# Kernel optimization log

Measured on AMD Instinct MI355X. Metric: run time of the kernel, lower is better.

## Reference

```python
import jax, jax.numpy as jnp
import numpy as np

N, E, B = 50000, 800000, 64
IN_C, HID, HEADS = 128, 64, 4
NEG_SLOPE = 0.2


def _gat_layer(x, src, dst, W, a_src, a_dst, bias, heads, out_c, concat):
    # x: [N, F_in] -> h: [N, heads, out_c]
    h = (x @ W).reshape(-1, heads, out_c)
    alpha_src = jnp.sum(h * a_src[None], axis=-1)  # [N, heads]
    alpha_dst = jnp.sum(h * a_dst[None], axis=-1)  # [N, heads]
    e = jax.nn.leaky_relu(alpha_src[src] + alpha_dst[dst], NEG_SLOPE)  # [Etot, heads]
    # segment softmax over incoming edges of each destination node
    m = jax.lax.stop_gradient(jax.ops.segment_max(e, dst, num_segments=N))
    m = jnp.where(jnp.isfinite(m), m, 0.0)
    ex = jnp.exp(e - m[dst])
    denom = jax.ops.segment_sum(ex, dst, num_segments=N)
    alpha = ex / jnp.maximum(denom[dst], 1e-16)
    msg = h[src] * alpha[:, :, None]  # [Etot, heads, out_c]
    out = jax.ops.segment_sum(msg, dst, num_segments=N)  # [N, heads, out_c]
    if concat:
        return out.reshape(-1, heads * out_c) + bias
    return out.mean(axis=1) + bias


def setup_inputs() -> dict:
    key = jax.random.key(0)
    ks = jax.random.split(key, 16)
    g = lambda k, shp, fan: jax.random.normal(k, shp, jnp.float32) * (1.0 / np.sqrt(fan))
    return {
        "x": jax.random.normal(ks[0], (N, IN_C), jnp.float32),
        "edge_index": jax.random.randint(ks[1], (2, E), 0, N, jnp.int64),
        "batch": jnp.sort(jax.random.randint(ks[2], (N,), 0, B, jnp.int64)),
        "W1": g(ks[3], (IN_C, HEADS * HID), IN_C),
        "as1": g(ks[4], (HEADS, HID), HID),
        "ad1": g(ks[5], (HEADS, HID), HID),
        "b1": jnp.zeros((HEADS * HID,), jnp.float32),
        "W2": g(ks[6], (HEADS * HID, HEADS * HID), HEADS * HID),
        "as2": g(ks[7], (HEADS, HID), HID),
        "ad2": g(ks[8], (HEADS, HID), HID),
        "b2": jnp.zeros((HID,), jnp.float32),
        "Wm1": g(ks[9], (HID, HID), HID),
        "bm1": jnp.zeros((HID,), jnp.float32),
        "Wm2": g(ks[10], (HID, 1), HID),
        "bm2": jnp.zeros((1,), jnp.float32),
    }


def reference(x, edge_index, batch, W1, as1, ad1, b1, W2, as2, ad2, b2, Wm1, bm1, Wm2, bm2):
    # add self loops (PyG GATConv default)
    loops = jnp.arange(N, dtype=edge_index.dtype)
    src = jnp.concatenate([edge_index[0], loops])
    dst = jnp.concatenate([edge_index[1], loops])
    h = _gat_layer(x, src, dst, W1, as1, ad1, b1, HEADS, HID, concat=True)
    h = jax.nn.relu(h)
    h = _gat_layer(h, src, dst, W2, as2, ad2, b2, HEADS, HID, concat=False)
    # global mean pool over graphs
    counts = jax.ops.segment_sum(jnp.ones((N,), h.dtype), batch, num_segments=B)
    pooled = jax.ops.segment_sum(h, batch, num_segments=B) / jnp.maximum(counts, 1.0)[:, None]
    # graph MLP
    out = jax.nn.relu(pooled @ Wm1 + bm1) @ Wm2 + bm2  # [B, 1]
    return out
```

## Files before the change

### kernel.cpp

```cpp
#include <hip/hip_runtime.h>
#include <hip/hip_bf16.h>

#define N_NODES 50000
#define N_EDGES 800000
#define ETOT    (N_EDGES + N_NODES)
#define NB      64
#define IN_C    128
#define HID     64
#define HEADS   4
#define F1      (HEADS * HID)
#define NEG     0.2f
#define SCAN_NBLK ((N_NODES + 255) / 256)

typedef __attribute__((ext_vector_type(8))) short  short8v;
typedef __attribute__((ext_vector_type(4))) float  float4v;

__device__ __forceinline__ float lrelu(float x) { return x >= 0.f ? x : NEG * x; }

__device__ __forceinline__ unsigned short f2bf(float f) {
    unsigned u = __float_as_uint(f);
    u += 0x7FFFu + ((u >> 16) & 1u);
    return (unsigned short)(u >> 16);
}
__device__ __forceinline__ float bf2f(unsigned short h) {
    return __uint_as_float(((unsigned)h) << 16);
}

__device__ __forceinline__ int wf_idx(int k, int n) {
    return (((k >> 5) * 16 + (n >> 4)) << 9) + (((k >> 3) & 3) << 7) + ((n & 15) << 3) + (k & 7);
}

__global__ void deg_kernel(const int* __restrict__ ei, int* __restrict__ deg,
                           const float* __restrict__ W1,
                           unsigned short* __restrict__ W1h, unsigned short* __restrict__ W1l,
                           const float* __restrict__ W2,
                           unsigned short* __restrict__ W2h, unsigned short* __restrict__ W2l) {
    int e = blockIdx.x * 256 + threadIdx.x;
    const int N1 = IN_C * 256;
    if (e < N1) {
        int k = e >> 8, n = e & 255;
        float v = W1[e];
        unsigned short h = f2bf(v);
        int idx = wf_idx(k, n);
        W1h[idx] = h;
        W1l[idx] = f2bf(v - bf2f(h));
    } else if (e < N1 + F1 * 256) {
        int j = e - N1;
        int k = j >> 8, n = j & 255;
        float v = W2[j];
        unsigned short h = f2bf(v);
        int idx = wf_idx(k, n);
        W2h[idx] = h;
        W2l[idx] = f2bf(v - bf2f(h));
    }
    if (e >= ETOT) return;
    int d = (e < N_EDGES) ? ei[N_EDGES + e] : (e - N_EDGES);
    atomicAdd(&deg[d], 1);
}

__global__ void scan1_kernel(const int* __restrict__ deg, int* __restrict__ part) {
    __shared__ int sh[256];
    int t = threadIdx.x;
    int i = blockIdx.x * 256 + t;
    sh[t] = (i < N_NODES) ? deg[i] : 0;
    __syncthreads();
    #pragma unroll
    for (int o = 128; o; o >>= 1) {
        if (t < o) sh[t] += sh[t + o];
        __syncthreads();
    }
    if (t == 0) part[blockIdx.x] = sh[0];
}

__global__ void scan2_kernel(int* __restrict__ part, int* __restrict__ off) {
    __shared__ int sh[256];
    int t = threadIdx.x;
    int v = (t < SCAN_NBLK) ? part[t] : 0;
    sh[t] = v;
    __syncthreads();
    #pragma unroll
    for (int o = 1; o < 256; o <<= 1) {
        int u = (t >= o) ? sh[t - o] : 0;
        __syncthreads();
        sh[t] += u;
        __syncthreads();
    }
    if (t < SCAN_NBLK) part[t] = sh[t] - v;
    if (t == 255) off[N_NODES] = sh[255];
}

__global__ void scan3_kernel(int* __restrict__ deg, const int* __restrict__ part,
                             int* __restrict__ off) {
    __shared__ int sh[256];
    int t = threadIdx.x;
    int i = blockIdx.x * 256 + t;
    int v = (i < N_NODES) ? deg[i] : 0;
    sh[t] = v;
    __syncthreads();
    #pragma unroll
    for (int o = 1; o < 256; o <<= 1) {
        int u = (t >= o) ? sh[t - o] : 0;
        __syncthreads();
        sh[t] += u;
        __syncthreads();
    }
    if (i < N_NODES) {
        off[i] = part[blockIdx.x] + sh[t] - v;
        deg[i] = 0;
    }
}

__global__ void scatter_kernel(const int* __restrict__ ei, const int* __restrict__ off,
                               int* __restrict__ cursor, int* __restrict__ esrc) {
    int e = blockIdx.x * 256 + threadIdx.x;
    if (e >= ETOT) return;
    int s, d;
    if (e < N_EDGES) { s = ei[e]; d = ei[N_EDGES + e]; }
    else             { s = d = e - N_EDGES; }
    int pos = off[d] + atomicAdd(&cursor[d], 1);
    esrc[pos] = s;
}

template <bool SPLIT_A, int K>
__global__ __launch_bounds__(256) void gemm_mfma(const float* __restrict__ Af32,
                                                 const unsigned short* __restrict__ Abg,
                                                 const unsigned short* __restrict__ Wfh,
                                                 const unsigned short* __restrict__ Wfl,
                                                 const float* __restrict__ a_s,
                                                 const float* __restrict__ a_d,
                                                 unsigned short* __restrict__ Cb,
                                                 float* __restrict__ asrcO,
                                                 float* __restrict__ adstO,
                                                 int M) {
    __shared__ float smc[32][260];
    int t  = threadIdx.x;
    int m0 = blockIdx.x * 64;
    int w  = t >> 6, l = t & 63;
    int lr = l & 15, lk = (l >> 4) * 8;

    float asv[4], adv[4];
    #pragma unroll
    for (int nf = 0; nf < 4; ++nf) {
        asv[nf] = a_s[w * 64 + nf * 16 + lr];
        adv[nf] = a_d[w * 64 + nf * 16 + lr];
    }

    float4v acc[4][4];
    #pragma unroll
    for (int mf = 0; mf < 4; ++mf)
        #pragma unroll
        for (int nf = 0; nf < 4; ++nf)
            acc[mf][nf] = (float4v){0.f, 0.f, 0.f, 0.f};

    constexpr int KB = K / 32;
    #pragma unroll 2
    for (int kb = 0; kb < KB; ++kb) {
        short8v b_hf[4], b_lf[4];
        #pragma unroll
        for (int nf = 0; nf < 4; ++nf) {
            size_t bidx = (size_t)((kb * 16 + w * 4 + nf) * 512 + l * 8);
            b_hf[nf] = *(const short8v*)&Wfh[bidx];
            b_lf[nf] = *(const short8v*)&Wfl[bidx];
        }
        short8v a_f[4];
        #pragma unroll
        for (int mf = 0; mf < 4; ++mf) {
            int gr = m0 + mf * 16 + lr;
            if (SPLIT_A) {
                float4 v0 = make_float4(0.f, 0.f, 0.f, 0.f), v1 = v0;
                if (gr < M) {
                    const float* ap = &Af32[(size_t)gr * K + kb * 32 + lk];
                    v0 = *(const float4*)ap;
                    v1 = *(const float4*)(ap + 4);
                }
                short8v a;
                a[0] = (short)f2bf(v0.x); a[1] = (short)f2bf(v0.y);
                a[2] = (short)f2bf(v0.z); a[3] = (short)f2bf(v0.w);
                a[4] = (short)f2bf(v1.x); a[5] = (short)f2bf(v1.y);
                a[6] = (short)f2bf(v1.z); a[7] = (short)f2bf(v1.w);
                a_f[mf] = a;
            } else {
                short8v a = {0,0,0,0,0,0,0,0};
                if (gr < M) a = *(const short8v*)&Abg[(size_t)gr * K + kb * 32 + lk];
                a_f[mf] = a;
            }
        }
        #pragma unroll
        for (int mf = 0; mf < 4; ++mf)
            #pragma unroll
            for (int nf = 0; nf < 4; ++nf) {
                acc[mf][nf] = __builtin_amdgcn_mfma_f32_16x16x32_bf16(a_f[mf], b_hf[nf], acc[mf][nf], 0, 0, 0);
                acc[mf][nf] = __builtin_amdgcn_mfma_f32_16x16x32_bf16(a_f[mf], b_lf[nf], acc[mf][nf], 0, 0, 0);
            }
    }

    #pragma unroll
    for (int mf = 0; mf < 4; ++mf)
        #pragma unroll
        for (int r = 0; r < 4; ++r) {
            float ps = acc[mf][0][r] * asv[0] + acc[mf][1][r] * asv[1]
                     + acc[mf][2][r] * asv[2] + acc[mf][3][r] * asv[3];
            float pd = acc[mf][0][r] * adv[0] + acc[mf][1][r] * adv[1]
                     + acc[mf][2][r] * adv[2] + acc[mf][3][r] * adv[3];
            #pragma unroll
            for (int o = 8; o; o >>= 1) {
                ps += __shfl_xor(ps, o);
                pd += __shfl_xor(pd, o);
            }
            int gr = m0 + mf * 16 + (l >> 4) * 4 + r;
            if (lr == 0 && gr < M) {
                asrcO[gr * 4 + w] = ps;
                adstO[gr * 4 + w] = pd;
            }
        }

    #pragma unroll
    for (int half = 0; half < 2; ++half) {
        __syncthreads();
        #pragma unroll
        for (int mf2 = 0; mf2 < 2; ++mf2) {
            int mf = half * 2 + mf2;
            #pragma unroll
            for (int nf = 0; nf < 4; ++nf)
                #pragma unroll
                for (int r = 0; r < 4; ++r)
                    smc[mf2 * 16 + (l >> 4) * 4 + r][w * 64 + nf * 16 + lr] = acc[mf][nf][r];
        }
        __syncthreads();
        #pragma unroll
        for (int p = 0; p < 8; ++p) {
            int idx = t + p * 256;
            int row = idx >> 6, c4 = (idx & 63) * 4;
            int gr = m0 + half * 32 + row;
            if (gr < M) {
                float4 v = *(const float4*)&smc[row][c4];
                ushort4 hv;
                hv.x = f2bf(v.x); hv.y = f2bf(v.y); hv.z = f2bf(v.z); hv.w = f2bf(v.w);
                *(ushort4*)&Cb[(size_t)gr * F1 + c4] = hv;
            }
        }
    }
}

template <int LAYER>
__global__ void agg_kernel(const unsigned short* __restrict__ hb,
                           const float* __restrict__ asrc,
                           const float* __restrict__ adst,
                           const int* __restrict__ off,
                           const int* __restrict__ esrc,
                           const float* __restrict__ bias,
                           float* __restrict__ outF,
                           unsigned short* __restrict__ oh) {
    __shared__ int   soff[64];
    __shared__ float cf[64][4];
    int d    = blockIdx.x;
    int lane = threadIdx.x;
    int w    = lane >> 4;
    int e0 = off[d], e1 = off[d + 1];
    float4 ad = *(const float4*)(adst + (size_t)d * 4);
    float den = 0.f;
    float a0 = 0.f, a1 = 0.f, a2 = 0.f, a3 = 0.f;
    const char* hbase = (const char*)hb;
    int lb = lane * 8;

    for (int base = e0; base < e1; base += 64) {
        int cnt = min(64, e1 - base);
        if (lane < cnt) {
            int s = esrc[base + lane];
            soff[lane] = s * (F1 * 2);
            float4 as = *(const float4*)(asrc + (size_t)s * 4);
            cf[lane][0] = __expf(lrelu(as.x + ad.x));
            cf[lane][1] = __expf(lrelu(as.y + ad.y));
            cf[lane][2] = __expf(lrelu(as.z + ad.z));
            cf[lane][3] = __expf(lrelu(as.w + ad.w));
        }
        __syncthreads();
        int i = 0;
        for (; i + 4 <= cnt; i += 4) {
            int o0 = soff[i], o1 = soff[i + 1], o2 = soff[i + 2], o3 = soff[i + 3];
            ushort4 h0 = *(const ushort4*)(hbase + o0 + lb);
            ushort4 h1 = *(const ushort4*)(hbase + o1 + lb);
            ushort4 h2 = *(const ushort4*)(hbase + o2 + lb);
            ushort4 h3 = *(const ushort4*)(hbase + o3 + lb);
            float c0 = cf[i][w], c1 = cf[i + 1][w], c2 = cf[i + 2][w], c3 = cf[i + 3][w];
            den += (c0 + c1) + (c2 + c3);
            a0 += c0 * bf2f(h0.x) + c1 * bf2f(h1.x) + c2 * bf2f(h2.x) + c3 * bf2f(h3.x);
            a1 += c0 * bf2f(h0.y) + c1 * bf2f(h1.y) + c2 * bf2f(h2.y) + c3 * bf2f(h3.y);
            a2 += c0 * bf2f(h0.z) + c1 * bf2f(h1.z) + c2 * bf2f(h2.z) + c3 * bf2f(h3.z);
            a3 += c0 * bf2f(h0.w) + c1 * bf2f(h1.w) + c2 * bf2f(h2.w) + c3 * bf2f(h3.w);
        }
        for (; i < cnt; ++i) {
            int o = soff[i];
            float c = cf[i][w];
            ushort4 hv = *(const ushort4*)(hbase + o + lb);
            den += c;
            a0 += c * bf2f(hv.x);
            a1 += c * bf2f(hv.y);
            a2 += c * bf2f(hv.z);
            a3 += c * bf2f(hv.w);
        }
        __syncthreads();
    }

    float r = 1.f / fmaxf(den, 1e-16f);
    if (LAYER == 1) {
        ushort4 hi;
        hi.x = f2bf(fmaxf(a0 * r + bias[lane * 4 + 0], 0.f));
        hi.y = f2bf(fmaxf(a1 * r + bias[lane * 4 + 1], 0.f));
        hi.z = f2bf(fmaxf(a2 * r + bias[lane * 4 + 2], 0.f));
        hi.w = f2bf(fmaxf(a3 * r + bias[lane * 4 + 3], 0.f));
        *(ushort4*)&oh[(size_t)d * F1 + lane * 4] = hi;
    } else {
        float v0 = a0 * r, v1 = a1 * r, v2 = a2 * r, v3 = a3 * r;
        v0 += __shfl_xor(v0, 16); v0 += __shfl_xor(v0, 32);
        v1 += __shfl_xor(v1, 16); v1 += __shfl_xor(v1, 32);
        v2 += __shfl_xor(v2, 16); v2 += __shfl_xor(v2, 32);
        v3 += __shfl_xor(v3, 16); v3 += __shfl_xor(v3, 32);
        if (lane < 16) {
            float4 o;
            o.x = 0.25f * v0 + bias[lane * 4 + 0];
            o.y = 0.25f * v1 + bias[lane * 4 + 1];
            o.z = 0.25f * v2 + bias[lane * 4 + 2];
            o.w = 0.25f * v3 + bias[lane * 4 + 3];
            *(float4*)&outF[(size_t)d * HID + lane * 4] = o;
        }
    }
}

__device__ __forceinline__ int lowerb(const int* __restrict__ a, int n, int v) {
    int lo = 0, hi = n;
    while (lo < hi) { int m = (lo + hi) >> 1; if (a[m] < v) lo = m + 1; else hi = m; }
    return lo;
}

__global__ void poolmlp_kernel(const float* __restrict__ h2,
                               const int* __restrict__ batch,
                               const float* __restrict__ Wm1, const float* __restrict__ bm1,
                               const float* __restrict__ Wm2, const float* __restrict__ bm2,
                               float* __restrict__ out) {
    __shared__ float sh[4][HID];
    int b = blockIdx.x;
    int t = threadIdx.x, w = t >> 6, c = t & 63;
    int lo = lowerb(batch, N_NODES, b);
    int hi = lowerb(batch, N_NODES, b + 1);
    float s = 0.f;
    for (int n = lo + w; n < hi; n += 4) s += h2[(size_t)n * HID + c];
    sh[w][c] = s;
    __syncthreads();
    if (w == 0) {
        float inv = 1.f / fmaxf((float)(hi - lo), 1.f);
        float P = (sh[0][c] + sh[1][c] + sh[2][c] + sh[3][c]) * inv;
        sh[0][c] = P;
        float s1 = bm1[c];
        #pragma unroll
        for (int k = 0; k < HID; ++k) s1 += sh[0][k] * Wm1[k * HID + c];
        float r = fmaxf(s1, 0.f) * Wm2[c];
        #pragma unroll
        for (int o = 32; o; o >>= 1) r += __shfl_xor(r, o);
        if (c == 0) out[b] = r + bm2[0];
    }
}

extern "C" void kernel_launch(void* const* d_in, const int* in_sizes, int n_in,
                              void* d_out, int out_size, void* d_ws, size_t ws_size,
                              hipStream_t stream) {
    const float* x   = (const float*)d_in[0];
    const int*   ei  = (const int*)d_in[1];
    const int*   bat = (const int*)d_in[2];
    const float* W1  = (const float*)d_in[3];
    const float* as1 = (const float*)d_in[4];
    const float* ad1 = (const float*)d_in[5];
    const float* b1  = (const float*)d_in[6];
    const float* W2  = (const float*)d_in[7];
    const float* as2 = (const float*)d_in[8];
    const float* ad2 = (const float*)d_in[9];
    const float* b2  = (const float*)d_in[10];
    const float* Wm1 = (const float*)d_in[11];
    const float* bm1 = (const float*)d_in[12];
    const float* Wm2 = (const float*)d_in[13];
    const float* bm2 = (const float*)d_in[14];
    float* out = (float*)d_out;

    char* ws = (char*)d_ws;
    size_t cursor = 0;
    auto alloc = [&](size_t bytes) {
        void* p = ws + cursor;
        cursor += (bytes + 511) & ~(size_t)511;
        return p;
    };
    int*   deg    = (int*)alloc((size_t)N_NODES * 4);
    int*   off    = (int*)alloc((size_t)(N_NODES + 1) * 4);
    int*   part   = (int*)alloc((size_t)SCAN_NBLK * 4);
    int*   esrc   = (int*)alloc((size_t)ETOT * 4);
    unsigned short* bufHb = (unsigned short*)alloc((size_t)N_NODES * F1 * 2);
    char*  U      = (char*)alloc((size_t)N_NODES * F1 * 4);
    unsigned short* oh = (unsigned short*)U;
    float* bufO   = (float*)U;
    float* asrc   = (float*)alloc((size_t)N_NODES * HEADS * 4);
    float* adst   = (float*)alloc((size_t)N_NODES * HEADS * 4);
    unsigned short* W1th = (unsigned short*)alloc((size_t)256 * IN_C * 2);
    unsigned short* W1tl = (unsigned short*)alloc((size_t)256 * IN_C * 2);
    unsigned short* W2th = (unsigned short*)alloc((size_t)256 * F1 * 2);
    unsigned short* W2tl = (unsigned short*)alloc((size_t)256 * F1 * 2);

    hipMemsetAsync(deg, 0, (size_t)N_NODES * 4, stream);

    deg_kernel<<<(ETOT + 255) / 256, 256, 0, stream>>>(ei, deg, W1, W1th, W1tl,
                                                       W2, W2th, W2tl);
    scan1_kernel<<<SCAN_NBLK, 256, 0, stream>>>(deg, part);
    scan2_kernel<<<1, 256, 0, stream>>>(part, off);
    scan3_kernel<<<SCAN_NBLK, 256, 0, stream>>>(deg, part, off);
    scatter_kernel<<<(ETOT + 255) / 256, 256, 0, stream>>>(ei, off, deg, esrc);

    const int GB = (N_NODES + 63) / 64;
    gemm_mfma<true, IN_C><<<GB, 256, 0, stream>>>(x, nullptr, W1th, W1tl,
                                                  as1, ad1, bufHb, asrc, adst, N_NODES);
    agg_kernel<1><<<N_NODES, 64, 0, stream>>>(bufHb, asrc, adst, off, esrc, b1,
                                              nullptr, oh);

    gemm_mfma<false, F1><<<GB, 256, 0, stream>>>(nullptr, oh, W2th, W2tl,
                                                 as2, ad2, bufHb, asrc, adst, N_NODES);
    agg_kernel<2><<<N_NODES, 64, 0, stream>>>(bufHb, asrc, adst, off, esrc, b2,
                                              bufO, nullptr);

    poolmlp_kernel<<<NB, 256, 0, stream>>>(bufO, bat, Wm1, bm1, Wm2, bm2, out);
}
```

Before: 341.9 us.

## Fuse layer-1 aggregation with layer-2 GEMM in one kernel

Layer-1 edge aggregation now runs in a kernel where each 256-thread block aggregates 16 destination nodes, four per wave, into an LDS tile. The block then runs the layer-2 bf16 MFMA GEMM and the attention-logit projection straight from that tile. This removes the global round trip of the layer-1 output and one kernel launch. In exchange, only 16 rows feed each GEMM tile, so the W2 fragments are reloaded per block, and the wave-local LDS fence replaces block barriers during aggregation.

```diff
diff --git a/kernel.cpp b/kernel.cpp
--- a/kernel.cpp
+++ b/kernel.cpp
@@ -24,6 +24,10 @@
 }
 __device__ __forceinline__ float bf2f(unsigned short h) {
     return __uint_as_float(((unsigned)h) << 16);
+}
+
+__device__ __forceinline__ void wave_lds_fence() {
+    asm volatile("s_waitcnt lgkmcnt(0)" ::: "memory");
 }
 
 __device__ __forceinline__ int wf_idx(int k, int n) {
@@ -121,9 +125,8 @@
     esrc[pos] = s;
 }
 
-template <bool SPLIT_A, int K>
+template <int K>
 __global__ __launch_bounds__(256) void gemm_mfma(const float* __restrict__ Af32,
-                                                 const unsigned short* __restrict__ Abg,
                                                  const unsigned short* __restrict__ Wfh,
                                                  const unsigned short* __restrict__ Wfl,
                                                  const float* __restrict__ a_s,
@@ -166,24 +169,18 @@
         #pragma unroll
         for (int mf = 0; mf < 4; ++mf) {
             int gr = m0 + mf * 16 + lr;
-            if (SPLIT_A) {
-                float4 v0 = make_float4(0.f, 0.f, 0.f, 0.f), v1 = v0;
-                if (gr < M) {
-                    const float* ap = &Af32[(size_t)gr * K + kb * 32 + lk];
-                    v0 = *(const float4*)ap;
-                    v1 = *(const float4*)(ap + 4);
-                }
-                short8v a;
-                a[0] = (short)f2bf(v0.x); a[1] = (short)f2bf(v0.y);
-                a[2] = (short)f2bf(v0.z); a[3] = (short)f2bf(v0.w);
-                a[4] = (short)f2bf(v1.x); a[5] = (short)f2bf(v1.y);
-                a[6] = (short)f2bf(v1.z); a[7] = (short)f2bf(v1.w);
-                a_f[mf] = a;
-            } else {
-                short8v a = {0,0,0,0,0,0,0,0};
-                if (gr < M) a = *(const short8v*)&Abg[(size_t)gr * K + kb * 32 + lk];
-                a_f[mf] = a;
-            }
+            float4 v0 = make_float4(0.f, 0.f, 0.f, 0.f), v1 = v0;
+            if (gr < M) {
+                const float* ap = &Af32[(size_t)gr * K + kb * 32 + lk];
+                v0 = *(const float4*)ap;
+                v1 = *(const float4*)(ap + 4);
+            }
+            short8v a;
+            a[0] = (short)f2bf(v0.x); a[1] = (short)f2bf(v0.y);
+            a[2] = (short)f2bf(v0.z); a[3] = (short)f2bf(v0.w);
+            a[4] = (short)f2bf(v1.x); a[5] = (short)f2bf(v1.y);
+            a[6] = (short)f2bf(v1.z); a[7] = (short)f2bf(v1.w);
+            a_f[mf] = a;
         }
         #pragma unroll
         for (int mf = 0; mf < 4; ++mf)
@@ -242,15 +239,149 @@
     }
 }
 
-template <int LAYER>
-__global__ void agg_kernel(const unsigned short* __restrict__ hb,
-                           const float* __restrict__ asrc,
-                           const float* __restrict__ adst,
-                           const int* __restrict__ off,
-                           const int* __restrict__ esrc,
-                           const float* __restrict__ bias,
-                           float* __restrict__ outF,
-                           unsigned short* __restrict__ oh) {
+__global__ __launch_bounds__(256) void agg1g2_kernel(
+        const unsigned short* __restrict__ hb,
+        const float* __restrict__ asrc, const float* __restrict__ adst,
+        const int* __restrict__ off, const int* __restrict__ esrc,
+        const float* __restrict__ b1,
+        const unsigned short* __restrict__ W2h, const unsigned short* __restrict__ W2l,
+        const float* __restrict__ as2, const float* __restrict__ ad2,
+        unsigned short* __restrict__ h2b,
+        float* __restrict__ asrc2, float* __restrict__ adst2) {
+    __shared__ unsigned short outT[16][264];
+    __shared__ float smc[16][260];
+    __shared__ int   soff[4][64];
+    __shared__ float cf[4][64][4];
+    int t  = threadIdx.x;
+    int wv = t >> 6, l = t & 63;
+    int lr = l & 15, lk = (l >> 4) * 8;
+    int hd = l >> 4;
+    int nb = blockIdx.x * 16;
+    const char* hbase = (const char*)hb;
+    int lb = l * 8;
+
+    #pragma unroll
+    for (int j = 0; j < 4; ++j) {
+        int d  = nb + wv * 4 + j;
+        int e0 = off[d], e1 = off[d + 1];
+        float4 ad = *(const float4*)(adst + (size_t)d * 4);
+        float den = 0.f, a0 = 0.f, a1 = 0.f, a2 = 0.f, a3 = 0.f;
+        for (int base = e0; base < e1; base += 64) {
+            int cnt = min(64, e1 - base);
+            if (l < cnt) {
+                int s = esrc[base + l];
+                soff[wv][l] = s * (F1 * 2);
+                float4 as = *(const float4*)(asrc + (size_t)s * 4);
+                cf[wv][l][0] = __expf(lrelu(as.x + ad.x));
+                cf[wv][l][1] = __expf(lrelu(as.y + ad.y));
+                cf[wv][l][2] = __expf(lrelu(as.z + ad.z));
+                cf[wv][l][3] = __expf(lrelu(as.w + ad.w));
+            }
+            wave_lds_fence();
+            int i = 0;
+            for (; i + 4 <= cnt; i += 4) {
+                int o0 = soff[wv][i], o1 = soff[wv][i + 1];
+                int o2 = soff[wv][i + 2], o3 = soff[wv][i + 3];
+                ushort4 h0 = *(const ushort4*)(hbase + o0 + lb);
+                ushort4 h1 = *(const ushort4*)(hbase + o1 + lb);
+                ushort4 h2 = *(const ushort4*)(hbase + o2 + lb);
+                ushort4 h3 = *(const ushort4*)(hbase + o3 + lb);
+                float c0 = cf[wv][i][hd], c1 = cf[wv][i + 1][hd];
+                float c2 = cf[wv][i + 2][hd], c3 = cf[wv][i + 3][hd];
+                den += (c0 + c1) + (c2 + c3);
+                a0 += c0 * bf2f(h0.x) + c1 * bf2f(h1.x) + c2 * bf2f(h2.x) + c3 * bf2f(h3.x);
+                a1 += c0 * bf2f(h0.y) + c1 * bf2f(h1.y) + c2 * bf2f(h2.y) + c3 * bf2f(h3.y);
+                a2 += c0 * bf2f(h0.z) + c1 * bf2f(h1.z) + c2 * bf2f(h2.z) + c3 * bf2f(h3.z);
+                a3 += c0 * bf2f(h0.w) + c1 * bf2f(h1.w) + c2 * bf2f(h2.w) + c3 * bf2f(h3.w);
+            }
+            for (; i < cnt; ++i) {
+                int o = soff[wv][i];
+                float c = cf[wv][i][hd];
+                ushort4 hv = *(const ushort4*)(hbase + o + lb);
+                den += c;
+                a0 += c * bf2f(hv.x);
+                a1 += c * bf2f(hv.y);
+                a2 += c * bf2f(hv.z);
+                a3 += c * bf2f(hv.w);
+            }
+            wave_lds_fence();
+        }
+        float r = 1.f / fmaxf(den, 1e-16f);
+        ushort4 hv;
+        hv.x = f2bf(fmaxf(a0 * r + b1[l * 4 + 0], 0.f));
+        hv.y = f2bf(fmaxf(a1 * r + b1[l * 4 + 1], 0.f));
+        hv.z = f2bf(fmaxf(a2 * r + b1[l * 4 + 2], 0.f));
+        hv.w = f2bf(fmaxf(a3 * r + b1[l * 4 + 3], 0.f));
+        *(ushort4*)&outT[wv * 4 + j][l * 4] = hv;
+    }
+    __syncthreads();
+
+    float asv[4], adv[4];
+    #pragma unroll
+    for (int nf = 0; nf < 4; ++nf) {
+        asv[nf] = as2[wv * 64 + nf * 16 + lr];
+        adv[nf] = ad2[wv * 64 + nf * 16 + lr];
+    }
+    float4v acc[4];
+    #pragma unroll
+    for (int nf = 0; nf < 4; ++nf) acc[nf] = (float4v){0.f, 0.f, 0.f, 0.f};
+
+    #pragma unroll
+    for (int kb = 0; kb < 8; ++kb) {
+        short8v a_f = *(short8v*)&outT[lr][kb * 32 + lk];
+        #pragma unroll
+        for (int nf = 0; nf < 4; ++nf) {
+            size_t bidx = (size_t)((kb * 16 + wv * 4 + nf) * 512 + l * 8);
+            short8v bh = *(const short8v*)&W2h[bidx];
+            short8v bl = *(const short8v*)&W2l[bidx];
+            acc[nf] = __builtin_amdgcn_mfma_f32_16x16x32_bf16(a_f, bh, acc[nf], 0, 0, 0);
+            acc[nf] = __builtin_amdgcn_mfma_f32_16x16x32_bf16(a_f, bl, acc[nf], 0, 0, 0);
+        }
+    }
+
+    #pragma unroll
+    for (int r = 0; r < 4; ++r) {
+        float ps = acc[0][r] * asv[0] + acc[1][r] * asv[1]
+                 + acc[2][r] * asv[2] + acc[3][r] * asv[3];
+        float pd = acc[0][r] * adv[0] + acc[1][r] * adv[1]
+                 + acc[2][r] * adv[2] + acc[3][r] * adv[3];
+        #pragma unroll
+        for (int o = 8; o; o >>= 1) {
+            ps += __shfl_xor(ps, o);
+            pd += __shfl_xor(pd, o);
+        }
+        if (lr == 0) {
+            int node = nb + (l >> 4) * 4 + r;
+            asrc2[node * 4 + wv] = ps;
+            adst2[node * 4 + wv] = pd;
+        }
+    }
+
+    __syncthreads();
+    #pragma unroll
+    for (int nf = 0; nf < 4; ++nf)
+        #pragma unroll
+        for (int r = 0; r < 4; ++r)
+            smc[(l >> 4) * 4 + r][wv * 64 + nf * 16 + lr] = acc[nf][r];
+    __syncthreads();
+    #pragma unroll
+    for (int p = 0; p < 4; ++p) {
+        int idx = t + p * 256;
+        int row = idx >> 6, c4 = (idx & 63) * 4;
+        float4 v = *(const float4*)&smc[row][c4];
+        ushort4 hv;
+        hv.x = f2bf(v.x); hv.y = f2bf(v.y); hv.z = f2bf(v.z); hv.w = f2bf(v.w);
+        *(ushort4*)&h2b[(size_t)(nb + row) * F1 + c4] = hv;
+    }
+}
+
+__global__ void agg2_kernel(const unsigned short* __restrict__ hb,
+                            const float* __restrict__ asrc,
+                            const float* __restrict__ adst,
+                            const int* __restrict__ off,
+                            const int* __restrict__ esrc,
+                            const float* __restrict__ bias,
+                            float* __restrict__ outF) {
     __shared__ int   soff[64];
     __shared__ float cf[64][4];
     int d    = blockIdx.x;
@@ -303,27 +434,18 @@
     }
 
     float r = 1.f / fmaxf(den, 1e-16f);
-    if (LAYER == 1) {
-        ushort4 hi;
-        hi.x = f2bf(fmaxf(a0 * r + bias[lane * 4 + 0], 0.f));
-        hi.y = f2bf(fmaxf(a1 * r + bias[lane * 4 + 1], 0.f));
-        hi.z = f2bf(fmaxf(a2 * r + bias[lane * 4 + 2], 0.f));
-        hi.w = f2bf(fmaxf(a3 * r + bias[lane * 4 + 3], 0.f));
-        *(ushort4*)&oh[(size_t)d * F1 + lane * 4] = hi;
-    } else {
-        float v0 = a0 * r, v1 = a1 * r, v2 = a2 * r, v3 = a3 * r;
-        v0 += __shfl_xor(v0, 16); v0 += __shfl_xor(v0, 32);
-        v1 += __shfl_xor(v1, 16); v1 += __shfl_xor(v1, 32);
-        v2 += __shfl_xor(v2, 16); v2 += __shfl_xor(v2, 32);
-        v3 += __shfl_xor(v3, 16); v3 += __shfl_xor(v3, 32);
-        if (lane < 16) {
-            float4 o;
-            o.x = 0.25f * v0 + bias[lane * 4 + 0];
-            o.y = 0.25f * v1 + bias[lane * 4 + 1];
-            o.z = 0.25f * v2 + bias[lane * 4 + 2];
-            o.w = 0.25f * v3 + bias[lane * 4 + 3];
-            *(float4*)&outF[(size_t)d * HID + lane * 4] = o;
-        }
+    float v0 = a0 * r, v1 = a1 * r, v2 = a2 * r, v3 = a3 * r;
+    v0 += __shfl_xor(v0, 16); v0 += __shfl_xor(v0, 32);
+    v1 += __shfl_xor(v1, 16); v1 += __shfl_xor(v1, 32);
+    v2 += __shfl_xor(v2, 16); v2 += __shfl_xor(v2, 32);
+    v3 += __shfl_xor(v3, 16); v3 += __shfl_xor(v3, 32);
+    if (lane < 16) {
+        float4 o;
+        o.x = 0.25f * v0 + bias[lane * 4 + 0];
+        o.y = 0.25f * v1 + bias[lane * 4 + 1];
+        o.z = 0.25f * v2 + bias[lane * 4 + 2];
+        o.w = 0.25f * v3 + bias[lane * 4 + 3];
+        *(float4*)&outF[(size_t)d * HID + lane * 4] = o;
     }
 }
 
@@ -393,11 +515,12 @@
     int*   part   = (int*)alloc((size_t)SCAN_NBLK * 4);
     int*   esrc   = (int*)alloc((size_t)ETOT * 4);
     unsigned short* bufHb = (unsigned short*)alloc((size_t)N_NODES * F1 * 2);
-    char*  U      = (char*)alloc((size_t)N_NODES * F1 * 4);
-    unsigned short* oh = (unsigned short*)U;
-    float* bufO   = (float*)U;
+    unsigned short* h2b   = (unsigned short*)alloc((size_t)N_NODES * F1 * 2);
+    float* bufO   = (float*)alloc((size_t)N_NODES * HID * 4);
     float* asrc   = (float*)alloc((size_t)N_NODES * HEADS * 4);
     float* adst   = (float*)alloc((size_t)N_NODES * HEADS * 4);
+    float* asrc2  = (float*)alloc((size_t)N_NODES * HEADS * 4);
+    float* adst2  = (float*)alloc((size_t)N_NODES * HEADS * 4);
     unsigned short* W1th = (unsigned short*)alloc((size_t)256 * IN_C * 2);
     unsigned short* W1tl = (unsigned short*)alloc((size_t)256 * IN_C * 2);
     unsigned short* W2th = (unsigned short*)alloc((size_t)256 * F1 * 2);
@@ -413,15 +536,12 @@
     scatter_kernel<<<(ETOT + 255) / 256, 256, 0, stream>>>(ei, off, deg, esrc);
 
     const int GB = (N_NODES + 63) / 64;
-    gemm_mfma<true, IN_C><<<GB, 256, 0, stream>>>(x, nullptr, W1th, W1tl,
-                                                  as1, ad1, bufHb, asrc, adst, N_NODES);
-    agg_kernel<1><<<N_NODES, 64, 0, stream>>>(bufHb, asrc, adst, off, esrc, b1,
-                                              nullptr, oh);
-
-    gemm_mfma<false, F1><<<GB, 256, 0, stream>>>(nullptr, oh, W2th, W2tl,
-                                                 as2, ad2, bufHb, asrc, adst, N_NODES);
-    agg_kernel<2><<<N_NODES, 64, 0, stream>>>(bufHb, asrc, adst, off, esrc, b2,
-                                              bufO, nullptr);
+    gemm_mfma<IN_C><<<GB, 256, 0, stream>>>(x, W1th, W1tl, as1, ad1,
+                                            bufHb, asrc, adst, N_NODES);
+    agg1g2_kernel<<<N_NODES / 16, 256, 0, stream>>>(bufHb, asrc, adst, off, esrc, b1,
+                                                    W2th, W2tl, as2, ad2,
+                                                    h2b, asrc2, adst2);
+    agg2_kernel<<<N_NODES, 64, 0, stream>>>(h2b, asrc2, adst2, off, esrc, b2, bufO);
 
     poolmlp_kernel<<<NB, 256, 0, stream>>>(bufO, bat, Wm1, bm1, Wm2, bm2, out);
 }
```

After: 335.5 us. Within noise of the previous version (-1.9%).
